# Kernel optimization log

Hardware: AMD Instinct MI355X
Metric: run time of the kernel (lower is better)

The kernel has to match this reference:

```python
import jax, jax.numpy as jnp
import numpy as np

TOP_K = 2

def setup_inputs() -> dict:
    key = jax.random.key(0)
    k0, k1, k2, k3, k4 = jax.random.split(key, 5)
    B, S, D, H, E = 2, 2048, 1024, 2048, 8
    x = jax.random.normal(k0, (B, S, D), dtype=jnp.float32)
    router_w = jax.random.normal(k1, (D, E), dtype=jnp.float32) * (1.0 / np.sqrt(D))
    wg = jax.random.normal(k2, (E, D, H), dtype=jnp.float32) * (1.0 / np.sqrt(D))
    wu = jax.random.normal(k3, (E, D, H), dtype=jnp.float32) * (1.0 / np.sqrt(D))
    wd = jax.random.normal(k4, (E, H, D), dtype=jnp.float32) * (1.0 / np.sqrt(H))
    return {"x": x, "router_w": router_w, "wg": wg, "wu": wu, "wd": wd}

def reference(x, router_w, wg, wu, wd):
    B, S, D = x.shape
    E = router_w.shape[1]
    xf = x.reshape(-1, D)                                   # [T, D]
    router_logits = xf @ router_w                           # [T, E]
    top_logits, top_idx = jax.lax.top_k(router_logits, TOP_K)
    top_w = jax.nn.softmax(top_logits, axis=-1)             # [T, k]
    # Dense combine weights: W[t, e] = routing weight if e in top-k of t, else 0.
    combine = jnp.sum(jax.nn.one_hot(top_idx, E, dtype=x.dtype) * top_w[..., None], axis=1)  # [T, E]
    # SwiGLU experts, computed for all tokens and masked by the combine weights
    # (mathematically identical to the gather/scatter form in the original).
    gate = jnp.einsum('td,edh->eth', xf, wg)                # [E, T, H]
    up = jnp.einsum('td,edh->eth', xf, wu)                  # [E, T, H]
    fused = jax.nn.silu(gate) * up                          # [E, T, H]
    expert_out = jnp.einsum('eth,ehd->etd', fused, wd)      # [E, T, D]
    y = jnp.einsum('etd,te->td', expert_out, combine)       # [T, D]
    return y.reshape(B, S, D)
```

## Files before the change

### kernel.cpp

```cpp
#include <hip/hip_runtime.h>
#include <hip/hip_bf16.h>

#define T_TOK 4096
#define DDIM  1024
#define HDIM  2048
#define NEXP  8

typedef __attribute__((ext_vector_type(4))) float f32x4;
typedef __attribute__((ext_vector_type(8))) short s16x8;
typedef __hip_bfloat16 bf16;

typedef const void __attribute__((address_space(1))) gvoid;
typedef void __attribute__((address_space(3))) svoid;

__device__ __forceinline__ void gload16(const void* g, void* l) {
    __builtin_amdgcn_global_load_lds((gvoid*)g, (svoid*)l, 16, 0, 0);
}

__global__ void router_cast_kernel(const float* __restrict__ x, const float* __restrict__ rw,
                                   int* __restrict__ r_e, float* __restrict__ r_w,
                                   bf16* __restrict__ xb) {
    int wave = threadIdx.x >> 6, lane = threadIdx.x & 63;
    int t = blockIdx.x * 4 + wave;
    const float* xr = x + (size_t)t * DDIM;
    bf16* xbr = xb + (size_t)t * DDIM;
    double acc[NEXP];
#pragma unroll
    for (int e = 0; e < NEXP; ++e) acc[e] = 0.0;
#pragma unroll
    for (int c = 0; c < 4; ++c) {
        int d = c * 256 + lane * 4;
        float4 v = *reinterpret_cast<const float4*>(xr + d);
        union { ushort4 u; bf16 h[4]; } o;
        o.h[0] = __float2bfloat16(v.x);
        o.h[1] = __float2bfloat16(v.y);
        o.h[2] = __float2bfloat16(v.z);
        o.h[3] = __float2bfloat16(v.w);
        *reinterpret_cast<ushort4*>(xbr + d) = o.u;
        const float* rw0 = rw + (size_t)d * NEXP;
#pragma unroll
        for (int j = 0; j < 4; ++j) {
            float xv = (&v.x)[j];
            const float* rwr = rw0 + j * NEXP;
#pragma unroll
            for (int e = 0; e < NEXP; ++e) acc[e] += (double)xv * (double)rwr[e];
        }
    }
#pragma unroll
    for (int e = 0; e < NEXP; ++e) {
#pragma unroll
        for (int off = 32; off > 0; off >>= 1) acc[e] += __shfl_down(acc[e], off);
    }
    if (lane == 0) {
        int i0 = 0; double v0 = acc[0];
#pragma unroll
        for (int e = 1; e < NEXP; ++e) if (acc[e] > v0) { v0 = acc[e]; i0 = e; }
        int i1 = -1; double v1 = -1e300;
#pragma unroll
        for (int e = 0; e < NEXP; ++e) { if (e == i0) continue; if (acc[e] > v1) { v1 = acc[e]; i1 = e; } }
        float w0 = 1.0f / (1.0f + expf((float)(v1 - v0)));
        float w1 = 1.0f - w0;
        r_e[2*t]   = i0; r_e[2*t+1] = i1;
        r_w[2*t]   = w0; r_w[2*t+1] = w1;
    }
}

__global__ void binning_kernel(const int* __restrict__ r_e, const float* __restrict__ r_w,
                               int* __restrict__ offs, int* __restrict__ list,
                               float* __restrict__ slot_w) {
    __shared__ int scnt[NEXP], scur[NEXP], soff[NEXP + 1];
    int tid = threadIdx.x;
    if (tid < NEXP) { scnt[tid] = 0; scur[tid] = 0; }
    __syncthreads();
    for (int i = tid; i < 2 * T_TOK; i += 512) atomicAdd(&scnt[r_e[i]], 1);
    __syncthreads();
    if (tid == 0) {
        int s = 0;
        for (int e = 0; e < NEXP; ++e) { soff[e] = s; s += scnt[e]; }
        soff[NEXP] = s;
    }
    __syncthreads();
    if (tid < NEXP + 1) offs[tid] = soff[tid];
    for (int i = tid; i < 2 * T_TOK; i += 512) {
        int e = r_e[i];
        int pos = atomicAdd(&scur[e], 1);
        int slot = soff[e] + pos;
        list[slot] = i >> 1;
        slot_w[slot] = r_w[i];
    }
}

__global__ void transpose_cast_kernel(const float* __restrict__ in, bf16* __restrict__ out,
                                      int R, int C, int rmul, int roff, size_t outE) {
    __shared__ bf16 tile[64][68];
    const float* inp = in + (size_t)blockIdx.z * R * C;
    bf16* outp = out + (size_t)blockIdx.z * outE;
    int r0 = blockIdx.x * 64, c0 = blockIdx.y * 64;
    int tid = threadIdx.x;
#pragma unroll
    for (int i = 0; i < 4; ++i) {
        int idx = i * 256 + tid;
        int r = idx >> 4, c4 = (idx & 15) * 4;
        float4 v = *reinterpret_cast<const float4*>(inp + (size_t)(r0 + r) * C + c0 + c4);
        tile[r][c4 + 0] = __float2bfloat16(v.x);
        tile[r][c4 + 1] = __float2bfloat16(v.y);
        tile[r][c4 + 2] = __float2bfloat16(v.z);
        tile[r][c4 + 3] = __float2bfloat16(v.w);
    }
    __syncthreads();
#pragma unroll
    for (int i = 0; i < 4; ++i) {
        int idx = i * 256 + tid;
        int c = idx >> 4, r4 = (idx & 15) * 4;
        union { ushort4 u; bf16 h[4]; } w;
        w.h[0] = tile[r4 + 0][c];
        w.h[1] = tile[r4 + 1][c];
        w.h[2] = tile[r4 + 2][c];
        w.h[3] = tile[r4 + 3][c];
        *reinterpret_cast<ushort4*>(outp + ((size_t)(c0 + c) * rmul + roff) * R + r0 + r4) = w.u;
    }
}

__global__ __launch_bounds__(256, 2)
void gateup_kernel(const bf16* __restrict__ xb, const bf16* __restrict__ wguT,
                   const int* __restrict__ offs, const int* __restrict__ list,
                   bf16* __restrict__ hbuf) {
    int e = blockIdx.z;
    int base = offs[e];
    int ne = offs[e + 1] - base;
    int m0 = blockIdx.y * 128;
    if (m0 >= ne) return;
    int n0 = blockIdx.x * 128;

    __shared__ bf16 As[2][8192];
    __shared__ bf16 Bs[2][8192];

    int tid = threadIdx.x, lane = tid & 63, wid = tid >> 6;
    int sub = tid >> 3;
    int koff = 8 * ((tid & 7) ^ (sub & 7));

    const bf16* bbase = wguT + (size_t)e * (2 * HDIM) * DDIM + (size_t)n0 * DDIM;

    const bf16* aS[4]; const bf16* bS[4];
    int dst[4];
#pragma unroll
    for (int i = 0; i < 4; ++i) {
        int row = i * 32 + sub;
        int r = m0 + row; if (r > ne - 1) r = ne - 1;
        aS[i] = xb + (size_t)list[base + r] * DDIM + koff;
        bS[i] = bbase + (size_t)row * DDIM + koff;
        dst[i] = (i * 32 + wid * 8) * 64;
    }

    int rl = lane & 15, kq = 8 * (lane >> 4);
    int wrow = (wid >> 1) * 64;
    int wcol = (wid & 1) * 64;
    int xorv = (rl & 7) * 8;

    f32x4 zero4 = {0.f, 0.f, 0.f, 0.f};
    f32x4 acc[4][4];
#pragma unroll
    for (int mi = 0; mi < 4; ++mi)
#pragma unroll
        for (int ni = 0; ni < 4; ++ni) acc[mi][ni] = zero4;

    const int nk = DDIM / 64;

#define GU_STAGE(tt, buf)                                     \
    {                                                         \
        int k0 = (tt) * 64;                                   \
        _Pragma("unroll")                                     \
        for (int i = 0; i < 4; ++i) {                         \
            gload16(aS[i] + k0, &As[buf][dst[i]]);            \
            gload16(bS[i] + k0, &Bs[buf][dst[i]]);            \
        }                                                     \
    }

    GU_STAGE(0, 0);
    GU_STAGE(1, 1);
    asm volatile("s_waitcnt vmcnt(8)" ::: "memory");
    __builtin_amdgcn_s_barrier();

    for (int t = 0; t < nk; ++t) {
        const bf16* Ab = As[t & 1];
        const bf16* Bb = Bs[t & 1];
#pragma unroll
        for (int kk = 0; kk < 2; ++kk) {
            int kos = (kk * 32 + kq) ^ xorv;
            s16x8 a[4], b[4];
#pragma unroll
            for (int mi = 0; mi < 4; ++mi)
                a[mi] = *reinterpret_cast<const s16x8*>(Ab + (wrow + mi * 16 + rl) * 64 + kos);
#pragma unroll
            for (int ni = 0; ni < 4; ++ni)
                b[ni] = *reinterpret_cast<const s16x8*>(Bb + (wcol + ni * 16 + rl) * 64 + kos);
            __builtin_amdgcn_s_setprio(1);
#pragma unroll
            for (int mi = 0; mi < 4; ++mi)
#pragma unroll
                for (int ni = 0; ni < 4; ++ni)
                    acc[mi][ni] = __builtin_amdgcn_mfma_f32_16x16x32_bf16(a[mi], b[ni], acc[mi][ni], 0, 0, 0);
            __builtin_amdgcn_s_setprio(0);
        }
        __builtin_amdgcn_sched_barrier(0);
        __builtin_amdgcn_s_barrier();
        if (t + 2 < nk) GU_STAGE(t + 2, t & 1);
        if (t + 1 < nk) {
            if (t + 2 < nk) asm volatile("s_waitcnt vmcnt(8)" ::: "memory");
            else            asm volatile("s_waitcnt vmcnt(0)" ::: "memory");
            __builtin_amdgcn_s_barrier();
        }
    }
#undef GU_STAGE

    int rbase = (lane >> 4) * 4, cbase = lane & 15;
    bool evenlane = (lane & 1) == 0;
#pragma unroll
    for (int mi = 0; mi < 4; ++mi) {
#pragma unroll
        for (int ni = 0; ni < 4; ++ni) {
#pragma unroll
            for (int r = 0; r < 4; ++r) {
                float own = acc[mi][ni][r];
                float oth = __shfl_xor(own, 1);
                int row = m0 + wrow + mi * 16 + rbase + r;
                if (evenlane && row < ne) {
                    float g = own, u = oth;
                    float h = (g / (1.0f + expf(-g))) * u;
                    int hcol = (n0 + wcol + ni * 16 + cbase) >> 1;
                    hbuf[(size_t)(base + row) * HDIM + hcol] = __float2bfloat16(h);
                }
            }
        }
    }
}

__global__ __launch_bounds__(256, 2)
void down_kernel(const bf16* __restrict__ hbuf, const bf16* __restrict__ wdT,
                 const int* __restrict__ offs, const int* __restrict__ list,
                 const float* __restrict__ slot_w, float* __restrict__ y) {
    int e = blockIdx.z;
    int base = offs[e];
    int ne = offs[e + 1] - base;
    int m0 = blockIdx.y * 128;
    if (m0 >= ne) return;
    int n0 = blockIdx.x * 128;

    __shared__ bf16 As[2][8192];
    __shared__ bf16 Bs[2][8192];

    int tid = threadIdx.x, lane = tid & 63, wid = tid >> 6;
    int sub = tid >> 3;
    int koff = 8 * ((tid & 7) ^ (sub & 7));

    const bf16* bbase = wdT + (size_t)e * DDIM * HDIM + (size_t)n0 * HDIM;

    const bf16* aS[4]; const bf16* bS[4];
    int dst[4];
#pragma unroll
    for (int i = 0; i < 4; ++i) {
        int row = i * 32 + sub;
        int r = m0 + row; if (r > ne - 1) r = ne - 1;
        aS[i] = hbuf + (size_t)(base + r) * HDIM + koff;
        bS[i] = bbase + (size_t)row * HDIM + koff;
        dst[i] = (i * 32 + wid * 8) * 64;
    }

    int rl = lane & 15, kq = 8 * (lane >> 4);
    int wrow = (wid >> 1) * 64;
    int wcol = (wid & 1) * 64;
    int xorv = (rl & 7) * 8;

    f32x4 zero4 = {0.f, 0.f, 0.f, 0.f};
    f32x4 acc[4][4];
#pragma unroll
    for (int mi = 0; mi < 4; ++mi)
#pragma unroll
        for (int ni = 0; ni < 4; ++ni) acc[mi][ni] = zero4;

    const int nk = HDIM / 64;

#define DN_STAGE(tt, buf)                                     \
    {                                                         \
        int k0 = (tt) * 64;                                   \
        _Pragma("unroll")                                     \
        for (int i = 0; i < 4; ++i) {                         \
            gload16(aS[i] + k0, &As[buf][dst[i]]);            \
            gload16(bS[i] + k0, &Bs[buf][dst[i]]);            \
        }                                                     \
    }

    DN_STAGE(0, 0);
    DN_STAGE(1, 1);
    asm volatile("s_waitcnt vmcnt(8)" ::: "memory");
    __builtin_amdgcn_s_barrier();

    for (int t = 0; t < nk; ++t) {
        const bf16* Ab = As[t & 1];
        const bf16* Bb = Bs[t & 1];
#pragma unroll
        for (int kk = 0; kk < 2; ++kk) {
            int kos = (kk * 32 + kq) ^ xorv;
            s16x8 a[4], b[4];
#pragma unroll
            for (int mi = 0; mi < 4; ++mi)
                a[mi] = *reinterpret_cast<const s16x8*>(Ab + (wrow + mi * 16 + rl) * 64 + kos);
#pragma unroll
            for (int ni = 0; ni < 4; ++ni)
                b[ni] = *reinterpret_cast<const s16x8*>(Bb + (wcol + ni * 16 + rl) * 64 + kos);
            __builtin_amdgcn_s_setprio(1);
#pragma unroll
            for (int mi = 0; mi < 4; ++mi)
#pragma unroll
                for (int ni = 0; ni < 4; ++ni)
                    acc[mi][ni] = __builtin_amdgcn_mfma_f32_16x16x32_bf16(a[mi], b[ni], acc[mi][ni], 0, 0, 0);
            __builtin_amdgcn_s_setprio(0);
        }
        __builtin_amdgcn_sched_barrier(0);
        __builtin_amdgcn_s_barrier();
        if (t + 2 < nk) DN_STAGE(t + 2, t & 1);
        if (t + 1 < nk) {
            if (t + 2 < nk) asm volatile("s_waitcnt vmcnt(8)" ::: "memory");
            else            asm volatile("s_waitcnt vmcnt(0)" ::: "memory");
            __builtin_amdgcn_s_barrier();
        }
    }
#undef DN_STAGE

    int rbase = (lane >> 4) * 4, cbase = lane & 15;
#pragma unroll
    for (int mi = 0; mi < 4; ++mi) {
#pragma unroll
        for (int r = 0; r < 4; ++r) {
            int row = m0 + wrow + mi * 16 + rbase + r;
            if (row < ne) {
                int slot = base + row;
                int tok = list[slot];
                float w = slot_w[slot];
                float* yrow = y + (size_t)tok * DDIM + n0 + wcol + cbase;
#pragma unroll
                for (int ni = 0; ni < 4; ++ni)
                    atomicAdd(yrow + ni * 16, w * acc[mi][ni][r]);
            }
        }
    }
}

extern "C" void kernel_launch(void* const* d_in, const int* in_sizes, int n_in,
                              void* d_out, int out_size, void* d_ws, size_t ws_size,
                              hipStream_t stream) {
    const float* x  = (const float*)d_in[0];
    const float* rw = (const float*)d_in[1];
    const float* wg = (const float*)d_in[2];
    const float* wu = (const float*)d_in[3];
    const float* wd = (const float*)d_in[4];
    float* y = (float*)d_out;

    char* ws = (char*)d_ws;
    int*   r_e    = (int*)  (ws + 0);
    float* r_w    = (float*)(ws + 32768);
    int*   offs   = (int*)  (ws + 65600);
    int*   list   = (int*)  (ws + 65664);
    float* slot_w = (float*)(ws + 98432);
    bf16*  xb     = (bf16*) (ws + 1048576ull);
    bf16*  wguT   = (bf16*) (ws + 16777216ull);
    bf16*  wdT    = (bf16*) (ws + 83886080ull);
    bf16*  hbuf   = (bf16*) (ws + 117440512ull);

    transpose_cast_kernel<<<dim3(DDIM / 64, HDIM / 64, NEXP), 256, 0, stream>>>(
        wg, wguT, DDIM, HDIM, 2, 0, (size_t)2 * HDIM * DDIM);
    transpose_cast_kernel<<<dim3(DDIM / 64, HDIM / 64, NEXP), 256, 0, stream>>>(
        wu, wguT, DDIM, HDIM, 2, 1, (size_t)2 * HDIM * DDIM);
    transpose_cast_kernel<<<dim3(HDIM / 64, DDIM / 64, NEXP), 256, 0, stream>>>(
        wd, wdT, HDIM, DDIM, 1, 0, (size_t)DDIM * HDIM);

    router_cast_kernel<<<dim3(T_TOK / 4), 256, 0, stream>>>(x, rw, r_e, r_w, xb);
    binning_kernel<<<dim3(1), 512, 0, stream>>>(r_e, r_w, offs, list, slot_w);

    hipMemsetAsync(d_out, 0, (size_t)out_size * sizeof(float), stream);

    gateup_kernel<<<dim3(2 * HDIM / 128, T_TOK / 128, NEXP), 256, 0, stream>>>(xb, wguT, offs, list, hbuf);
    down_kernel<<<dim3(DDIM / 128, T_TOK / 128, NEXP), 256, 0, stream>>>(hbuf, wdT, offs, list, slot_w, y);
}
```

Baseline: 296.8 us.

## Halve K-tile to 32 with new swizzled LDS layout to raise occupancy

Both grouped GEMM kernels now stage K-tiles of 32 instead of 64. This halves the LDS footprint per block to 32 KB, and launch bounds are raised to allow 5 blocks per CU. A new paired-row XOR swizzle layout and precomputed fragment offsets keep the LDS reads conflict-free with the narrower tile. The cost is twice as many barrier and wait iterations per K loop and less MFMA work between synchronisations, which could offset the latency hiding gained from higher occupancy.

New measurement: 521.9 us. 75.8% more time.

```diff
diff --git a/kernel.cpp b/kernel.cpp
--- a/kernel.cpp
+++ b/kernel.cpp
@@ -15,6 +15,12 @@
 
 __device__ __forceinline__ void gload16(const void* g, void* l) {
     __builtin_amdgcn_global_load_lds((gvoid*)g, (svoid*)l, 16, 0, 0);
+}
+
+__device__ __forceinline__ int frag_off(int rr, int kq) {
+    int lr = rr >> 1;
+    int ch = ((rr & 1) << 2) + (kq >> 3);
+    return lr * 64 + (ch ^ (lr & 7)) * 8;
 }
 
 __global__ void router_cast_kernel(const float* __restrict__ x, const float* __restrict__ rw,
@@ -121,7 +127,7 @@
     }
 }
 
-__global__ __launch_bounds__(256, 2)
+__global__ __launch_bounds__(256, 5)
 void gateup_kernel(const bf16* __restrict__ xb, const bf16* __restrict__ wguT,
                    const int* __restrict__ offs, const int* __restrict__ list,
                    bf16* __restrict__ hbuf) {
@@ -132,30 +138,36 @@
     if (m0 >= ne) return;
     int n0 = blockIdx.x * 128;
 
-    __shared__ bf16 As[2][8192];
-    __shared__ bf16 Bs[2][8192];
+    __shared__ bf16 As[2][4096];
+    __shared__ bf16 Bs[2][4096];
 
     int tid = threadIdx.x, lane = tid & 63, wid = tid >> 6;
-    int sub = tid >> 3;
-    int koff = 8 * ((tid & 7) ^ (sub & 7));
 
     const bf16* bbase = wguT + (size_t)e * (2 * HDIM) * DDIM + (size_t)n0 * DDIM;
 
-    const bf16* aS[4]; const bf16* bS[4];
-    int dst[4];
-#pragma unroll
-    for (int i = 0; i < 4; ++i) {
-        int row = i * 32 + sub;
-        int r = m0 + row; if (r > ne - 1) r = ne - 1;
-        aS[i] = xb + (size_t)list[base + r] * DDIM + koff;
-        bS[i] = bbase + (size_t)row * DDIM + koff;
-        dst[i] = (i * 32 + wid * 8) * 64;
+    const bf16* aS[2]; const bf16* bS[2];
+    int sdst[2];
+#pragma unroll
+    for (int j = 0; j < 2; ++j) {
+        int q = wid + j * 4;
+        int lr = q * 8 + (lane >> 3);
+        int ch = (lane & 7) ^ (lr & 7);
+        int rr = 2 * lr + (ch >> 2);
+        int koff = (ch & 3) * 8;
+        int r = m0 + rr; if (r > ne - 1) r = ne - 1;
+        aS[j] = xb + (size_t)list[base + r] * DDIM + koff;
+        bS[j] = bbase + (size_t)rr * DDIM + koff;
+        sdst[j] = q * 512;
     }
 
     int rl = lane & 15, kq = 8 * (lane >> 4);
     int wrow = (wid >> 1) * 64;
     int wcol = (wid & 1) * 64;
-    int xorv = (rl & 7) * 8;
+    int offA[4], offB[4];
+#pragma unroll
+    for (int mi = 0; mi < 4; ++mi) offA[mi] = frag_off(wrow + mi * 16 + rl, kq);
+#pragma unroll
+    for (int ni = 0; ni < 4; ++ni) offB[ni] = frag_off(wcol + ni * 16 + rl, kq);
 
     f32x4 zero4 = {0.f, 0.f, 0.f, 0.f};
     f32x4 acc[4][4];
@@ -164,49 +176,42 @@
 #pragma unroll
         for (int ni = 0; ni < 4; ++ni) acc[mi][ni] = zero4;
 
-    const int nk = DDIM / 64;
+    const int nk = DDIM / 32;
 
 #define GU_STAGE(tt, buf)                                     \
     {                                                         \
-        int k0 = (tt) * 64;                                   \
-        _Pragma("unroll")                                     \
-        for (int i = 0; i < 4; ++i) {                         \
-            gload16(aS[i] + k0, &As[buf][dst[i]]);            \
-            gload16(bS[i] + k0, &Bs[buf][dst[i]]);            \
-        }                                                     \
+        int k0 = (tt) * 32;                                   \
+        gload16(aS[0] + k0, &As[buf][sdst[0]]);               \
+        gload16(aS[1] + k0, &As[buf][sdst[1]]);               \
+        gload16(bS[0] + k0, &Bs[buf][sdst[0]]);               \
+        gload16(bS[1] + k0, &Bs[buf][sdst[1]]);               \
     }
 
     GU_STAGE(0, 0);
     GU_STAGE(1, 1);
-    asm volatile("s_waitcnt vmcnt(8)" ::: "memory");
+    asm volatile("s_waitcnt vmcnt(4)" ::: "memory");
     __builtin_amdgcn_s_barrier();
 
     for (int t = 0; t < nk; ++t) {
         const bf16* Ab = As[t & 1];
         const bf16* Bb = Bs[t & 1];
-#pragma unroll
-        for (int kk = 0; kk < 2; ++kk) {
-            int kos = (kk * 32 + kq) ^ xorv;
-            s16x8 a[4], b[4];
-#pragma unroll
-            for (int mi = 0; mi < 4; ++mi)
-                a[mi] = *reinterpret_cast<const s16x8*>(Ab + (wrow + mi * 16 + rl) * 64 + kos);
+        s16x8 a[4], b[4];
+#pragma unroll
+        for (int mi = 0; mi < 4; ++mi) a[mi] = *reinterpret_cast<const s16x8*>(Ab + offA[mi]);
+#pragma unroll
+        for (int ni = 0; ni < 4; ++ni) b[ni] = *reinterpret_cast<const s16x8*>(Bb + offB[ni]);
+        __builtin_amdgcn_s_setprio(1);
+#pragma unroll
+        for (int mi = 0; mi < 4; ++mi)
 #pragma unroll
             for (int ni = 0; ni < 4; ++ni)
-                b[ni] = *reinterpret_cast<const s16x8*>(Bb + (wcol + ni * 16 + rl) * 64 + kos);
-            __builtin_amdgcn_s_setprio(1);
-#pragma unroll
-            for (int mi = 0; mi < 4; ++mi)
-#pragma unroll
-                for (int ni = 0; ni < 4; ++ni)
-                    acc[mi][ni] = __builtin_amdgcn_mfma_f32_16x16x32_bf16(a[mi], b[ni], acc[mi][ni], 0, 0, 0);
-            __builtin_amdgcn_s_setprio(0);
-        }
+                acc[mi][ni] = __builtin_amdgcn_mfma_f32_16x16x32_bf16(a[mi], b[ni], acc[mi][ni], 0, 0, 0);
+        __builtin_amdgcn_s_setprio(0);
         __builtin_amdgcn_sched_barrier(0);
         __builtin_amdgcn_s_barrier();
         if (t + 2 < nk) GU_STAGE(t + 2, t & 1);
         if (t + 1 < nk) {
-            if (t + 2 < nk) asm volatile("s_waitcnt vmcnt(8)" ::: "memory");
+            if (t + 2 < nk) asm volatile("s_waitcnt vmcnt(4)" ::: "memory");
             else            asm volatile("s_waitcnt vmcnt(0)" ::: "memory");
             __builtin_amdgcn_s_barrier();
         }
@@ -235,7 +240,7 @@
     }
 }
 
-__global__ __launch_bounds__(256, 2)
+__global__ __launch_bounds__(256, 5)
 void down_kernel(const bf16* __restrict__ hbuf, const bf16* __restrict__ wdT,
                  const int* __restrict__ offs, const int* __restrict__ list,
                  const float* __restrict__ slot_w, float* __restrict__ y) {
@@ -246,30 +251,36 @@
     if (m0 >= ne) return;
     int n0 = blockIdx.x * 128;
 
-    __shared__ bf16 As[2][8192];
-    __shared__ bf16 Bs[2][8192];
+    __shared__ bf16 As[2][4096];
+    __shared__ bf16 Bs[2][4096];
 
     int tid = threadIdx.x, lane = tid & 63, wid = tid >> 6;
-    int sub = tid >> 3;
-    int koff = 8 * ((tid & 7) ^ (sub & 7));
 
     const bf16* bbase = wdT + (size_t)e * DDIM * HDIM + (size_t)n0 * HDIM;
 
-    const bf16* aS[4]; const bf16* bS[4];
-    int dst[4];
-#pragma unroll
-    for (int i = 0; i < 4; ++i) {
-        int row = i * 32 + sub;
-        int r = m0 + row; if (r > ne - 1) r = ne - 1;
-        aS[i] = hbuf + (size_t)(base + r) * HDIM + koff;
-        bS[i] = bbase + (size_t)row * HDIM + koff;
-        dst[i] = (i * 32 + wid * 8) * 64;
+    const bf16* aS[2]; const bf16* bS[2];
+    int sdst[2];
+#pragma unroll
+    for (int j = 0; j < 2; ++j) {
+        int q = wid + j * 4;
+        int lr = q * 8 + (lane >> 3);
+        int ch = (lane & 7) ^ (lr & 7);
+        int rr = 2 * lr + (ch >> 2);
+        int koff = (ch & 3) * 8;
+        int r = m0 + rr; if (r > ne - 1) r = ne - 1;
+        aS[j] = hbuf + (size_t)(base + r) * HDIM + koff;
+        bS[j] = bbase + (size_t)rr * HDIM + koff;
+        sdst[j] = q * 512;
     }
 
     int rl = lane & 15, kq = 8 * (lane >> 4);
     int wrow = (wid >> 1) * 64;
     int wcol = (wid & 1) * 64;
-    int xorv = (rl & 7) * 8;
+    int offA[4], offB[4];
+#pragma unroll
+    for (int mi = 0; mi < 4; ++mi) offA[mi] = frag_off(wrow + mi * 16 + rl, kq);
+#pragma unroll
+    for (int ni = 0; ni < 4; ++ni) offB[ni] = frag_off(wcol + ni * 16 + rl, kq);
 
     f32x4 zero4 = {0.f, 0.f, 0.f, 0.f};
     f32x4 acc[4][4];
@@ -278,49 +289,42 @@
 #pragma unroll
         for (int ni = 0; ni < 4; ++ni) acc[mi][ni] = zero4;
 
-    const int nk = HDIM / 64;
+    const int nk = HDIM / 32;
 
 #define DN_STAGE(tt, buf)                                     \
     {                                                         \
-        int k0 = (tt) * 64;                                   \
-        _Pragma("unroll")                                     \
-        for (int i = 0; i < 4; ++i) {                         \
-            gload16(aS[i] + k0, &As[buf][dst[i]]);            \
-            gload16(bS[i] + k0, &Bs[buf][dst[i]]);            \
-        }                                                     \
+        int k0 = (tt) * 32;                                   \
+        gload16(aS[0] + k0, &As[buf][sdst[0]]);               \
+        gload16(aS[1] + k0, &As[buf][sdst[1]]);               \
+        gload16(bS[0] + k0, &Bs[buf][sdst[0]]);               \
+        gload16(bS[1] + k0, &Bs[buf][sdst[1]]);               \
     }
 
     DN_STAGE(0, 0);
     DN_STAGE(1, 1);
-    asm volatile("s_waitcnt vmcnt(8)" ::: "memory");
+    asm volatile("s_waitcnt vmcnt(4)" ::: "memory");
     __builtin_amdgcn_s_barrier();
 
     for (int t = 0; t < nk; ++t) {
         const bf16* Ab = As[t & 1];
         const bf16* Bb = Bs[t & 1];
-#pragma unroll
-        for (int kk = 0; kk < 2; ++kk) {
-            int kos = (kk * 32 + kq) ^ xorv;
-            s16x8 a[4], b[4];
-#pragma unroll
-            for (int mi = 0; mi < 4; ++mi)
-                a[mi] = *reinterpret_cast<const s16x8*>(Ab + (wrow + mi * 16 + rl) * 64 + kos);
+        s16x8 a[4], b[4];
+#pragma unroll
+        for (int mi = 0; mi < 4; ++mi) a[mi] = *reinterpret_cast<const s16x8*>(Ab + offA[mi]);
+#pragma unroll
+        for (int ni = 0; ni < 4; ++ni) b[ni] = *reinterpret_cast<const s16x8*>(Bb + offB[ni]);
+        __builtin_amdgcn_s_setprio(1);
+#pragma unroll
+        for (int mi = 0; mi < 4; ++mi)
 #pragma unroll
             for (int ni = 0; ni < 4; ++ni)
-                b[ni] = *reinterpret_cast<const s16x8*>(Bb + (wcol + ni * 16 + rl) * 64 + kos);
-            __builtin_amdgcn_s_setprio(1);
-#pragma unroll
-            for (int mi = 0; mi < 4; ++mi)
-#pragma unroll
-                for (int ni = 0; ni < 4; ++ni)
-                    acc[mi][ni] = __builtin_amdgcn_mfma_f32_16x16x32_bf16(a[mi], b[ni], acc[mi][ni], 0, 0, 0);
-            __builtin_amdgcn_s_setprio(0);
-        }
+                acc[mi][ni] = __builtin_amdgcn_mfma_f32_16x16x32_bf16(a[mi], b[ni], acc[mi][ni], 0, 0, 0);
+        __builtin_amdgcn_s_setprio(0);
         __builtin_amdgcn_sched_barrier(0);
         __builtin_amdgcn_s_barrier();
         if (t + 2 < nk) DN_STAGE(t + 2, t & 1);
         if (t + 1 < nk) {
-            if (t + 2 < nk) asm volatile("s_waitcnt vmcnt(8)" ::: "memory");
+            if (t + 2 < nk) asm volatile("s_waitcnt vmcnt(4)" ::: "memory");
             else            asm volatile("s_waitcnt vmcnt(0)" ::: "memory");
             __builtin_amdgcn_s_barrier();
         }
```
